# Performance work log

Hardware: AMD Instinct MI355X
Metric: run time of the kernel (lower is better)

## Reference

```python
import jax, jax.numpy as jnp
import numpy as np

B, L, D = 32, 128, 256  # batch, len_arg, in_dim (== h_dim)
H4 = 4 * D


def setup_inputs() -> dict:
    key = jax.random.key(0)
    k1, k2, k3, k4, k5, k6 = jax.random.split(key, 6)
    arg_1 = jax.random.normal(k1, (B, L, D), dtype=jnp.float32)
    arg_2 = jax.random.normal(k2, (B, L, D), dtype=jnp.float32)
    length_x1 = jax.random.randint(k3, (B,), 1, L + 1, dtype=jnp.int32)
    length_x2 = jax.random.randint(k4, (B,), 1, L + 1, dtype=jnp.int32)
    # xavier-normal-ish params
    fc_w = jax.random.normal(k5, (H4, D), dtype=jnp.float32) * (2.0 / (D + H4)) ** 0.5
    fc_b = jnp.zeros((H4,), dtype=jnp.float32)
    we_w = jax.random.normal(k6, (D,), dtype=jnp.float32) * (2.0 / (D + 1)) ** 0.5
    return {"arg_1": arg_1, "length_x1": length_x1, "arg_2": arg_2,
            "length_x2": length_x2, "fc_w": fc_w, "fc_b": fc_b, "we_w": we_w}


def reference(arg_1, length_x1, arg_2, length_x2, fc_w, fc_b, we_w):
    b, l, d = arg_1.shape
    # pairwise offsets: word_1[i] - word_2[j] -> [B, L, L, D]
    offset = arg_1[:, :, None, :] - arg_2[:, None, :, :]
    # validity mask replaces the per-sample pack+zero-pad (order inside dim 1 is
    # irrelevant: softmax + weighted-sum are permutation invariant, pads are 0)
    idx = jnp.arange(l)
    valid = (idx[None, :, None] < length_x1[:, None, None]) & \
            (idx[None, None, :] < length_x2[:, None, None])          # [B, L, L]
    matrix = jnp.where(valid[..., None], offset, 0.0).reshape(b, l * l, d)
    we = jnp.einsum('bnd,d->bn', matrix, we_w)                        # [B, L*L]
    we_masked = jnp.where(jnp.abs(we) < 1e-7, jnp.float32(-1e7), we)  # masked_fill
    alpha = jax.nn.softmax(we_masked, axis=1)                         # [B, L*L]
    pooled = jnp.einsum('bn,bnd->bd', alpha, matrix)                  # [B, D]
    out = jnp.tanh(pooled @ fc_w.T + fc_b)                            # [B, 4D]
    # dropout(0.5) is identity in eval mode
    return out
```

## Files before the change

### kernel.cpp

```cpp
#include <hip/hip_runtime.h>
#include <math.h>

#define BB 32
#define LL 128
#define DD 256
#define HH 1024
#define A1STRIDE 65

__device__ __forceinline__ float waveReduceSum(float v) {
#pragma unroll
    for (int m = 32; m >= 1; m >>= 1) v += __shfl_xor(v, m, 64);
    return v;
}

__global__ __launch_bounds__(1024) void batch_oct_kernel(
    const float* __restrict__ a1, const int* __restrict__ len1,
    const float* __restrict__ a2, const int* __restrict__ len2,
    const float* __restrict__ fcw, const float* __restrict__ fcb,
    const float* __restrict__ ww, float* __restrict__ out)
{
    const int blk  = blockIdx.x;
    const int b    = blk & 31;
    const int q8   = blk >> 5;
    const int tid  = threadIdx.x;
    const int wave = tid >> 6;
    const int lane = tid & 63;

    __shared__ __align__(16) float4 A1l[LL * A1STRIDE];
    __shared__ __align__(16) float4 part4[1024];
    __shared__ __align__(16) float4 wws4[DD / 4];
    __shared__ float s1[LL], s2[LL], E1[LL], E2m[LL];
    __shared__ float rsv[LL], csv[LL];
    __shared__ float redS[16], redM[16];
    __shared__ __align__(16) float4 ps4[DD / 4];

    const int l1 = len1[b];
    const int l2 = len2[b];

    if (tid < DD / 4) wws4[tid] = ((const float4*)ww)[tid];
    __syncthreads();

    const float* __restrict__ A1 = a1 + (size_t)b * LL * DD;
    const float* __restrict__ A2 = a2 + (size_t)b * LL * DD;

    {
        const int r = tid >> 2;
        const int t = tid & 3;
        float ax = 0.f, ay = 0.f, az = 0.f, aw = 0.f;
        if (r < LL) {
            const float4* __restrict__ row = (const float4*)(A1 + (size_t)r * DD);
#pragma unroll
            for (int qq = 0; qq < 16; ++qq) {
                const int idx = qq * 4 + t;
                const float4 v = row[idx];
                A1l[r * A1STRIDE + idx] = v;
                const float4 w = wws4[idx];
                ax += v.x * w.x; ay += v.y * w.y; az += v.z * w.z; aw += v.w * w.w;
            }
        } else {
            const float4* __restrict__ row = (const float4*)(A2 + (size_t)(r - LL) * DD);
#pragma unroll
            for (int qq = 0; qq < 16; ++qq) {
                const int idx = qq * 4 + t;
                const float4 v = row[idx];
                const float4 w = wws4[idx];
                ax += v.x * w.x; ay += v.y * w.y; az += v.z * w.z; aw += v.w * w.w;
            }
        }
        float s = (ax + ay) + (az + aw);
        s += __shfl_xor(s, 1, 64);
        s += __shfl_xor(s, 2, 64);
        if (t == 0) { if (r < LL) s1[r] = s; else s2[r - LL] = s; }
    }
    __syncthreads();

    {
        float v = 0.f;
        if (tid < LL) {
            const float e = expf(s1[tid]);
            E1[tid] = e;
            if (tid < l1) v = e;
        } else if (tid < 2 * LL) {
            const int j = tid - LL;
            const float e = expf(-s2[j]);
            E2m[j] = e;
            if (j < l2) v = e;
        }
        v = waveReduceSum(v);
        if (lane == 0) redS[wave] = v;
    }
    __syncthreads();

    {
        const int rr  = tid >> 2;
        const int sub = tid & 3;
        int c = 0;
        if (rr < LL) {
            if (rr < l1) {
                const float si = s1[rr];
                for (int j = sub; j < l2; j += 4)
                    if (fabsf(si - s2[j]) < 1e-7f) c++;
            }
        } else {
            const int jj = rr - LL;
            if (jj < l2) {
                const float sj = s2[jj];
                for (int i = sub; i < l1; i += 4)
                    if (fabsf(s1[i] - sj) < 1e-7f) c++;
            }
        }
        c += __shfl_xor(c, 1, 64);
        c += __shfl_xor(c, 2, 64);
        if (sub == 0) {
            if (rr < LL) rsv[rr] = (float)c;
            else         csv[rr - LL] = (float)c;
        }
    }
    __syncthreads();

    {
        float mc = (tid < LL && tid < l1) ? rsv[tid] : 0.f;
        mc = waveReduceSum(mc);
        if (lane == 0) redM[wave] = mc;
    }
    __syncthreads();
    const float S1 = redS[0] + redS[1];
    const float S2 = redS[2] + redS[3];
    const float Mtot = redM[0] + redM[1];
    const float dinv = 1.0f / (S1 * S2 - Mtot);

    if (tid < LL)
        rsv[tid] = (tid < l1) ? (E1[tid] * S2 - rsv[tid]) * dinv : 0.f;
    else if (tid < 2 * LL) {
        const int j = tid - LL;
        csv[j] = (j < l2) ? (E2m[j] * S1 - csv[j]) * dinv : 0.f;
    }
    __syncthreads();

    {
        const int d4 = tid & 63;
        const int g  = tid >> 6;
        const float4* __restrict__ A2v = (const float4*)A2;
        float4 acc = make_float4(0.f, 0.f, 0.f, 0.f);
#pragma unroll
        for (int k = 0; k < 8; ++k) {
            const int i = g * 8 + k;
            const float4 va = A1l[i * A1STRIDE + d4];
            const float4 vb = A2v[i * 64 + d4];
            const float r_ = rsv[i], c_ = csv[i];
            acc.x += r_ * va.x - c_ * vb.x;
            acc.y += r_ * va.y - c_ * vb.y;
            acc.z += r_ * va.z - c_ * vb.z;
            acc.w += r_ * va.w - c_ * vb.w;
        }
        part4[tid] = acc;
    }
    __syncthreads();
    if (tid < 256) {
        float4 p = part4[tid];
        const float4 p1 = part4[256 + tid];
        const float4 p2 = part4[512 + tid];
        const float4 p3 = part4[768 + tid];
        p.x += p1.x + p2.x + p3.x;
        p.y += p1.y + p2.y + p3.y;
        p.z += p1.z + p2.z + p3.z;
        p.w += p1.w + p2.w + p3.w;
        part4[tid] = p;
    }
    __syncthreads();
    if (tid < 64) {
        float4 p = part4[tid];
        const float4 p1 = part4[64 + tid];
        const float4 p2 = part4[128 + tid];
        const float4 p3 = part4[192 + tid];
        p.x += p1.x + p2.x + p3.x;
        p.y += p1.y + p2.y + p3.y;
        p.z += p1.z + p2.z + p3.z;
        p.w += p1.w + p2.w + p3.w;
        ps4[tid] = p;
    }
    __syncthreads();

    {
        const int hl  = tid >> 4;
        const int t16 = tid & 15;
        const float4 u0 = ps4[t16];
        const float4 u1 = ps4[16 + t16];
        const float4 u2 = ps4[32 + t16];
        const float4 u3 = ps4[48 + t16];
        float* __restrict__ outb = out + (size_t)b * HH;
#pragma unroll
        for (int pass = 0; pass < 2; ++pass) {
            const int h = q8 * 128 + pass * 64 + hl;
            const float4* __restrict__ wrow = (const float4*)(fcw + (size_t)h * DD);
            const float4 v0 = wrow[t16];
            const float4 v1 = wrow[16 + t16];
            const float4 v2 = wrow[32 + t16];
            const float4 v3 = wrow[48 + t16];
            float acc = v0.x * u0.x + v0.y * u0.y + v0.z * u0.z + v0.w * u0.w;
            acc      += v1.x * u1.x + v1.y * u1.y + v1.z * u1.z + v1.w * u1.w;
            acc      += v2.x * u2.x + v2.y * u2.y + v2.z * u2.z + v2.w * u2.w;
            acc      += v3.x * u3.x + v3.y * u3.y + v3.z * u3.z + v3.w * u3.w;
            acc += __shfl_xor(acc, 1, 64);
            acc += __shfl_xor(acc, 2, 64);
            acc += __shfl_xor(acc, 4, 64);
            acc += __shfl_xor(acc, 8, 64);
            if (t16 == 0) outb[h] = tanhf(acc + fcb[h]);
        }
    }
}

extern "C" void kernel_launch(void* const* d_in, const int* in_sizes, int n_in,
                              void* d_out, int out_size, void* d_ws, size_t ws_size,
                              hipStream_t stream) {
    const float* a1   = (const float*)d_in[0];
    const int*   len1 = (const int*)d_in[1];
    const float* a2   = (const float*)d_in[2];
    const int*   len2 = (const int*)d_in[3];
    const float* fcw  = (const float*)d_in[4];
    const float* fcb  = (const float*)d_in[5];
    const float* ww   = (const float*)d_in[6];
    float* out = (float*)d_out;

    batch_oct_kernel<<<256, 1024, 0, stream>>>(a1, len1, a2, len2, fcw, fcb, ww, out);
}
```

Measured before the change: 14.17 us.

## Keep A1/A2 rows in registers instead of LDS staging and re-reading A2

Each wave now loads 8 rows of both A1 and A2 into registers once. It computes the we_w dot products with full-wave shuffle reductions, then reuses the same registers for the weighted pooling sum. This removes the large LDS buffer for A1 (~133KB) and the second global read of A2. The cost is many more live registers per thread (32 float4) and 96 shuffles per thread for the reductions, which may cause spills under the 1024-thread launch bound.

```diff
diff --git a/kernel.cpp b/kernel.cpp
--- a/kernel.cpp
+++ b/kernel.cpp
@@ -5,7 +5,6 @@
 #define LL 128
 #define DD 256
 #define HH 1024
-#define A1STRIDE 65
 
 __device__ __forceinline__ float waveReduceSum(float v) {
 #pragma unroll
@@ -13,7 +12,7 @@
     return v;
 }
 
-__global__ __launch_bounds__(1024) void batch_oct_kernel(
+__global__ __launch_bounds__(1024) void batch_reg_kernel(
     const float* __restrict__ a1, const int* __restrict__ len1,
     const float* __restrict__ a2, const int* __restrict__ len2,
     const float* __restrict__ fcw, const float* __restrict__ fcb,
@@ -26,7 +25,6 @@
     const int wave = tid >> 6;
     const int lane = tid & 63;
 
-    __shared__ __align__(16) float4 A1l[LL * A1STRIDE];
     __shared__ __align__(16) float4 part4[1024];
     __shared__ __align__(16) float4 wws4[DD / 4];
     __shared__ float s1[LL], s2[LL], E1[LL], E2m[LL];
@@ -40,37 +38,62 @@
     if (tid < DD / 4) wws4[tid] = ((const float4*)ww)[tid];
     __syncthreads();
 
-    const float* __restrict__ A1 = a1 + (size_t)b * LL * DD;
-    const float* __restrict__ A2 = a2 + (size_t)b * LL * DD;
-
-    {
-        const int r = tid >> 2;
-        const int t = tid & 3;
-        float ax = 0.f, ay = 0.f, az = 0.f, aw = 0.f;
-        if (r < LL) {
-            const float4* __restrict__ row = (const float4*)(A1 + (size_t)r * DD);
-#pragma unroll
-            for (int qq = 0; qq < 16; ++qq) {
-                const int idx = qq * 4 + t;
-                const float4 v = row[idx];
-                A1l[r * A1STRIDE + idx] = v;
-                const float4 w = wws4[idx];
-                ax += v.x * w.x; ay += v.y * w.y; az += v.z * w.z; aw += v.w * w.w;
-            }
-        } else {
-            const float4* __restrict__ row = (const float4*)(A2 + (size_t)(r - LL) * DD);
-#pragma unroll
-            for (int qq = 0; qq < 16; ++qq) {
-                const int idx = qq * 4 + t;
-                const float4 v = row[idx];
-                const float4 w = wws4[idx];
-                ax += v.x * w.x; ay += v.y * w.y; az += v.z * w.z; aw += v.w * w.w;
-            }
-        }
-        float s = (ax + ay) + (az + aw);
-        s += __shfl_xor(s, 1, 64);
-        s += __shfl_xor(s, 2, 64);
-        if (t == 0) { if (r < LL) s1[r] = s; else s2[r - LL] = s; }
+    const float4* __restrict__ A1v = (const float4*)(a1 + (size_t)b * LL * DD);
+    const float4* __restrict__ A2v = (const float4*)(a2 + (size_t)b * LL * DD);
+
+    const int r0 = wave * 8;
+    const float4 w4 = wws4[lane];
+
+    float4 va0 = A1v[(r0 + 0) * 64 + lane];
+    float4 va1 = A1v[(r0 + 1) * 64 + lane];
+    float4 va2 = A1v[(r0 + 2) * 64 + lane];
+    float4 va3 = A1v[(r0 + 3) * 64 + lane];
+    float4 va4 = A1v[(r0 + 4) * 64 + lane];
+    float4 va5 = A1v[(r0 + 5) * 64 + lane];
+    float4 va6 = A1v[(r0 + 6) * 64 + lane];
+    float4 va7 = A1v[(r0 + 7) * 64 + lane];
+    float4 vb0 = A2v[(r0 + 0) * 64 + lane];
+    float4 vb1 = A2v[(r0 + 1) * 64 + lane];
+    float4 vb2 = A2v[(r0 + 2) * 64 + lane];
+    float4 vb3 = A2v[(r0 + 3) * 64 + lane];
+    float4 vb4 = A2v[(r0 + 4) * 64 + lane];
+    float4 vb5 = A2v[(r0 + 5) * 64 + lane];
+    float4 vb6 = A2v[(r0 + 6) * 64 + lane];
+    float4 vb7 = A2v[(r0 + 7) * 64 + lane];
+
+    {
+        float d1[8], d2[8];
+        d1[0] = va0.x * w4.x + va0.y * w4.y + va0.z * w4.z + va0.w * w4.w;
+        d1[1] = va1.x * w4.x + va1.y * w4.y + va1.z * w4.z + va1.w * w4.w;
+        d1[2] = va2.x * w4.x + va2.y * w4.y + va2.z * w4.z + va2.w * w4.w;
+        d1[3] = va3.x * w4.x + va3.y * w4.y + va3.z * w4.z + va3.w * w4.w;
+        d1[4] = va4.x * w4.x + va4.y * w4.y + va4.z * w4.z + va4.w * w4.w;
+        d1[5] = va5.x * w4.x + va5.y * w4.y + va5.z * w4.z + va5.w * w4.w;
+        d1[6] = va6.x * w4.x + va6.y * w4.y + va6.z * w4.z + va6.w * w4.w;
+        d1[7] = va7.x * w4.x + va7.y * w4.y + va7.z * w4.z + va7.w * w4.w;
+        d2[0] = vb0.x * w4.x + vb0.y * w4.y + vb0.z * w4.z + vb0.w * w4.w;
+        d2[1] = vb1.x * w4.x + vb1.y * w4.y + vb1.z * w4.z + vb1.w * w4.w;
+        d2[2] = vb2.x * w4.x + vb2.y * w4.y + vb2.z * w4.z + vb2.w * w4.w;
+        d2[3] = vb3.x * w4.x + vb3.y * w4.y + vb3.z * w4.z + vb3.w * w4.w;
+        d2[4] = vb4.x * w4.x + vb4.y * w4.y + vb4.z * w4.z + vb4.w * w4.w;
+        d2[5] = vb5.x * w4.x + vb5.y * w4.y + vb5.z * w4.z + vb5.w * w4.w;
+        d2[6] = vb6.x * w4.x + vb6.y * w4.y + vb6.z * w4.z + vb6.w * w4.w;
+        d2[7] = vb7.x * w4.x + vb7.y * w4.y + vb7.z * w4.z + vb7.w * w4.w;
+#pragma unroll
+        for (int m = 32; m >= 1; m >>= 1) {
+#pragma unroll
+            for (int k = 0; k < 8; ++k) {
+                d1[k] += __shfl_xor(d1[k], m, 64);
+                d2[k] += __shfl_xor(d2[k], m, 64);
+            }
+        }
+        if (lane == 0) {
+#pragma unroll
+            for (int k = 0; k < 8; ++k) {
+                s1[r0 + k] = d1[k];
+                s2[r0 + k] = d2[k];
+            }
+        }
     }
     __syncthreads();
 
@@ -138,21 +161,32 @@
     __syncthreads();
 
     {
-        const int d4 = tid & 63;
-        const int g  = tid >> 6;
-        const float4* __restrict__ A2v = (const float4*)A2;
         float4 acc = make_float4(0.f, 0.f, 0.f, 0.f);
-#pragma unroll
-        for (int k = 0; k < 8; ++k) {
-            const int i = g * 8 + k;
-            const float4 va = A1l[i * A1STRIDE + d4];
-            const float4 vb = A2v[i * 64 + d4];
-            const float r_ = rsv[i], c_ = csv[i];
-            acc.x += r_ * va.x - c_ * vb.x;
-            acc.y += r_ * va.y - c_ * vb.y;
-            acc.z += r_ * va.z - c_ * vb.z;
-            acc.w += r_ * va.w - c_ * vb.w;
-        }
+        float r_, c_;
+        r_ = rsv[r0 + 0]; c_ = csv[r0 + 0];
+        acc.x += r_ * va0.x - c_ * vb0.x; acc.y += r_ * va0.y - c_ * vb0.y;
+        acc.z += r_ * va0.z - c_ * vb0.z; acc.w += r_ * va0.w - c_ * vb0.w;
+        r_ = rsv[r0 + 1]; c_ = csv[r0 + 1];
+        acc.x += r_ * va1.x - c_ * vb1.x; acc.y += r_ * va1.y - c_ * vb1.y;
+        acc.z += r_ * va1.z - c_ * vb1.z; acc.w += r_ * va1.w - c_ * vb1.w;
+        r_ = rsv[r0 + 2]; c_ = csv[r0 + 2];
+        acc.x += r_ * va2.x - c_ * vb2.x; acc.y += r_ * va2.y - c_ * vb2.y;
+        acc.z += r_ * va2.z - c_ * vb2.z; acc.w += r_ * va2.w - c_ * vb2.w;
+        r_ = rsv[r0 + 3]; c_ = csv[r0 + 3];
+        acc.x += r_ * va3.x - c_ * vb3.x; acc.y += r_ * va3.y - c_ * vb3.y;
+        acc.z += r_ * va3.z - c_ * vb3.z; acc.w += r_ * va3.w - c_ * vb3.w;
+        r_ = rsv[r0 + 4]; c_ = csv[r0 + 4];
+        acc.x += r_ * va4.x - c_ * vb4.x; acc.y += r_ * va4.y - c_ * vb4.y;
+        acc.z += r_ * va4.z - c_ * vb4.z; acc.w += r_ * va4.w - c_ * vb4.w;
+        r_ = rsv[r0 + 5]; c_ = csv[r0 + 5];
+        acc.x += r_ * va5.x - c_ * vb5.x; acc.y += r_ * va5.y - c_ * vb5.y;
+        acc.z += r_ * va5.z - c_ * vb5.z; acc.w += r_ * va5.w - c_ * vb5.w;
+        r_ = rsv[r0 + 6]; c_ = csv[r0 + 6];
+        acc.x += r_ * va6.x - c_ * vb6.x; acc.y += r_ * va6.y - c_ * vb6.y;
+        acc.z += r_ * va6.z - c_ * vb6.z; acc.w += r_ * va6.w - c_ * vb6.w;
+        r_ = rsv[r0 + 7]; c_ = csv[r0 + 7];
+        acc.x += r_ * va7.x - c_ * vb7.x; acc.y += r_ * va7.y - c_ * vb7.y;
+        acc.z += r_ * va7.z - c_ * vb7.z; acc.w += r_ * va7.w - c_ * vb7.w;
         part4[tid] = acc;
     }
     __syncthreads();
@@ -222,5 +256,5 @@
     const float* ww   = (const float*)d_in[6];
     float* out = (float*)d_out;
 
-    batch_oct_kernel<<<256, 1024, 0, stream>>>(a1, len1, a2, len2, fcw, fcb, ww, out);
+    batch_reg_kernel<<<256, 1024, 0, stream>>>(a1, len1, a2, len2, fcw, fcb, ww, out);
 }
```

After: 16.29 us. +14.9%, slower.
